# Performance work log

Measured on AMD Instinct MI355X. Metric: run time of the kernel, lower is better.

## Reference

```python
import jax, jax.numpy as jnp
import numpy as np

B, T, E, H, D_PRICE = 16, 2048, 128, 4, 512


def setup_inputs() -> dict:
    key = jax.random.key(0)
    ks = jax.random.split(key, 22)
    f32 = jnp.float32

    def w(k, shape):
        fan_in = shape[0]
        return (jax.random.normal(k, shape, f32) / np.sqrt(fan_in)).astype(f32)

    def b(k, n):
        return (jax.random.normal(k, (n,), f32) * 0.01).astype(f32)

    inp = {
        # OHLC prices, positive, normalized scale
        "ohlc": jax.random.uniform(ks[0], (B, T, 4), f32, 0.5, 1.5),
        # ohlc_proj: Linear(4, 64)
        "Wp": w(ks[1], (4, 64)), "bp": b(ks[2], 64),
        # curvature_net: Linear(64,128) -> ReLU -> Linear(128,32)
        "Wc1": w(ks[3], (64, 128)), "bc1": b(ks[4], 128),
        "Wc2": w(ks[5], (128, 32)), "bc2": b(ks[6], 32),
        # volatility_net: Linear(64,64) -> ReLU -> Linear(64,16)
        "Wv1": w(ks[7], (64, 64)), "bv1": b(ks[8], 64),
        "Wv2": w(ks[9], (64, 16)), "bv2": b(ks[10], 16),
        # sr_field_net: Linear(64,64) -> ReLU -> Linear(64,16)
        "Ws1": w(ks[11], (64, 64)), "bs1": b(ks[12], 64),
        "Ws2": w(ks[13], (64, 16)), "bs2": b(ks[14], 16),
        # MultiheadAttention(embed_dim=128, num_heads=4): fused in-proj + out-proj
        "Wqkv": w(ks[15], (E, 3 * E)), "bqkv": b(ks[16], 3 * E),
        "Wo": w(ks[17], (E, E)), "bo": b(ks[18], E),
        # output_proj: Linear(128, d_price)
        "Wout": w(ks[19], (E, D_PRICE)), "bout": b(ks[20], D_PRICE),
    }
    return inp


def _mlp(x, W1, b1, W2, b2):
    return jax.nn.relu(x @ W1 + b1) @ W2 + b2


def reference(ohlc, Wp, bp, Wc1, bc1, Wc2, bc2, Wv1, bv1, Wv2, bv2,
              Ws1, bs1, Ws2, bs2, Wqkv, bqkv, Wo, bo, Wout, bout):
    # NB: compute_curvature / compute_volatility_surface / detect_sr_levels
    # in the original forward are dead code (results never used), so they are
    # omitted here; output math is identical.
    e = ohlc @ Wp + bp                                   # [B,T,64]
    feats = jnp.concatenate([
        e,
        _mlp(e, Wc1, bc1, Wc2, bc2),                     # [B,T,32]
        _mlp(e, Wv1, bv1, Wv2, bv2),                     # [B,T,16]
        _mlp(e, Ws1, bs1, Ws2, bs2),                     # [B,T,16]
    ], axis=-1)                                          # [B,T,128]

    Bn, Tn, En = feats.shape
    dh = En // H
    qkv = feats @ Wqkv + bqkv                            # [B,T,3E]
    q, k, v = jnp.split(qkv, 3, axis=-1)

    def heads(x):
        return x.reshape(Bn, Tn, H, dh).transpose(0, 2, 1, 3)  # [B,H,T,dh]

    q, k, v = heads(q), heads(k), heads(v)
    scores = jnp.einsum('bhqd,bhkd->bhqk', q, k) / np.sqrt(dh).astype(feats.dtype)
    a = jax.nn.softmax(scores, axis=-1)                  # [B,H,T,T]
    o = jnp.einsum('bhqk,bhkd->bhqd', a, v)
    o = o.transpose(0, 2, 1, 3).reshape(Bn, Tn, En)
    attended = o @ Wo + bo                               # [B,T,128]

    pooled = attended.mean(axis=1)                       # [B,128]
    return pooled @ Wout + bout                          # [B,512]
```

## Files before the change

kernel.cpp:

```cpp
#include <hip/hip_runtime.h>


typedef __attribute__((ext_vector_type(4)))  float f32x4;
typedef __attribute__((ext_vector_type(4)))  short short4v;
typedef __attribute__((ext_vector_type(8)))  short short8v;

static __device__ __forceinline__ unsigned short f2b(float f) {
    unsigned int u = __builtin_bit_cast(unsigned int, f);
    u += 0x7fffu + ((u >> 16) & 1u);
    return (unsigned short)(u >> 16);
}

static __device__ __forceinline__ unsigned int cvtpk_bf16(float a, float b) {
    unsigned int r;
    asm volatile("v_cvt_pk_bf16_f32 %0, %1, %2" : "=v"(r) : "v"(a), "v"(b));
    return r;
}

__global__ __launch_bounds__(256) void prep_kernel(
    const float* Wqkv, const float* Wc1, const float* Wc2, const float* Wv1,
    const float* Wv2, const float* Ws1, const float* Ws2,
    unsigned short* wqkvt, unsigned short* wc1t, unsigned short* wc2t,
    unsigned short* wv1t, unsigned short* wv2t, unsigned short* ws1t,
    unsigned short* ws2t, float* pooled, float* qkmax)
{
    int tid = threadIdx.x;
    if (blockIdx.x < 48) {
        __shared__ float tile[32][33];
        int bidn = blockIdx.x % 12, bidk = blockIdx.x / 12;
        int n0 = bidn * 32, k0 = bidk * 32;
        {
            int r = tid >> 3, cq = tid & 7;
            float4 v = *(const float4*)(Wqkv + (size_t)(k0 + r) * 384 + n0 + cq * 4);
            tile[r][cq*4+0] = v.x; tile[r][cq*4+1] = v.y;
            tile[r][cq*4+2] = v.z; tile[r][cq*4+3] = v.w;
        }
        __syncthreads();
        {
            int nr = tid >> 3, kq = tid & 7;
            union { unsigned short us[4]; short4v v; } pk;
#pragma unroll
            for (int j = 0; j < 4; ++j) pk.us[j] = f2b(tile[kq*4+j][nr]);
            *(short4v*)(wqkvt + (size_t)(n0 + nr) * 128 + k0 + kq * 4) = pk.v;
        }
        return;
    }
    int idx = (blockIdx.x - 48) * 256 + tid;
    if (idx < 8192)  { int n = idx >> 6, kk = idx & 63;  wc1t[idx] = f2b(Wc1[kk*128 + n]); return; }
    idx -= 8192;
    if (idx < 4096)  { int n = idx >> 7, kk = idx & 127; wc2t[idx] = f2b(Wc2[kk*32  + n]); return; }
    idx -= 4096;
    if (idx < 4096)  { int n = idx >> 6, kk = idx & 63;  wv1t[idx] = f2b(Wv1[kk*64  + n]); return; }
    idx -= 4096;
    if (idx < 1024)  { int n = idx >> 6, kk = idx & 63;  wv2t[idx] = f2b(Wv2[kk*16  + n]); return; }
    idx -= 1024;
    if (idx < 4096)  { int n = idx >> 6, kk = idx & 63;  ws1t[idx] = f2b(Ws1[kk*64  + n]); return; }
    idx -= 4096;
    if (idx < 1024)  { int n = idx >> 6, kk = idx & 63;  ws2t[idx] = f2b(Ws2[kk*16  + n]); return; }
    idx -= 1024;
    if (idx < 2048)  { pooled[idx] = 0.f; return; }
    idx -= 2048;
    if (idx < 128)   qkmax[idx] = 0.f;
}

template<int N, int K, int A_ROWB, int D_ROWB, bool RELU, bool TO_LDS>
static __device__ __forceinline__ void tile_gemm(
    const char* As, const unsigned short* __restrict__ BT,
    const float* __restrict__ bias, char* dst,
    unsigned short* __restrict__ gOut, int ocol,
    int m0, int w, int lane)
{
    constexpr int ASL = A_ROWB / 16, DSL = D_ROWB / 16;
    constexpr int NT = N / 16, KS = K / 32;
    int l15 = lane & 15, hi4 = lane >> 4;
    f32x4 acc[NT];
#pragma unroll
    for (int nt = 0; nt < NT; ++nt)
#pragma unroll
        for (int r = 0; r < 4; ++r) acc[nt][r] = 0.f;

#pragma unroll
    for (int ks = 0; ks < KS; ++ks) {
        int slot = ks * 4 + hi4;
        int m = w * 16 + l15;
        short8v af = *(const short8v*)(As + m * A_ROWB + ((slot ^ (m & (ASL - 1))) << 4));
#pragma unroll
        for (int nt = 0; nt < NT; ++nt) {
            int n = nt * 16 + l15;
            short8v bf = *(const short8v*)(BT + (size_t)n * K + slot * 8);
            acc[nt] = __builtin_amdgcn_mfma_f32_16x16x32_bf16(af, bf, acc[nt], 0, 0, 0);
        }
    }
#pragma unroll
    for (int nt = 0; nt < NT; ++nt) {
        int n = nt * 16 + l15;
        float bv = bias[n];
#pragma unroll
        for (int r = 0; r < 4; ++r) {
            int m = w * 16 + hi4 * 4 + r;
            float v = acc[nt][r] + bv;
            if (RELU) v = fmaxf(v, 0.f);
            if (TO_LDS) {
                int col = n;
                *(unsigned short*)(dst + m * D_ROWB + (((col >> 3) ^ (m & (DSL - 1))) << 4) + (col & 7) * 2) = f2b(v);
            } else {
                gOut[(size_t)(m0 + m) * 128 + ocol + n] = f2b(v);
            }
        }
    }
}

__global__ __launch_bounds__(256) void fused_mlp(
    const float* __restrict__ ohlc, const float* __restrict__ Wp, const float* __restrict__ bp,
    const unsigned short* __restrict__ wc1t, const float* __restrict__ bc1,
    const unsigned short* __restrict__ wc2t, const float* __restrict__ bc2,
    const unsigned short* __restrict__ wv1t, const float* __restrict__ bv1,
    const unsigned short* __restrict__ wv2t, const float* __restrict__ bv2,
    const unsigned short* __restrict__ ws1t, const float* __restrict__ bs1,
    const unsigned short* __restrict__ ws2t, const float* __restrict__ bs2,
    unsigned short* __restrict__ feats)
{
    __shared__ float wp[256];
    __shared__ float bpl[64];
    __shared__ char Et[64 * 128];
    __shared__ char Ht[64 * 256];

    int tid = threadIdx.x;
    int m0 = blockIdx.x * 64;
    int branch = blockIdx.y;
    wp[tid] = Wp[tid];
    if (tid < 64) bpl[tid] = bp[tid];
    __syncthreads();

    {
        int tok = tid >> 2, jq = tid & 3;
        float4 ov = ((const float4*)ohlc)[m0 + tok];
#pragma unroll
        for (int c = 0; c < 2; ++c) {
            int sl = jq * 2 + c;
            union { unsigned short us[8]; short8v v; } pk;
#pragma unroll
            for (int jj = 0; jj < 8; ++jj) {
                int j = sl * 8 + jj;
                float e = bpl[j] + ov.x * wp[j] + ov.y * wp[64 + j]
                                 + ov.z * wp[128 + j] + ov.w * wp[192 + j];
                pk.us[jj] = f2b(e);
            }
            *(short8v*)(Et + tok * 128 + ((sl ^ (tok & 7)) << 4)) = pk.v;
            if (branch == 0)
                *(short8v*)(feats + (size_t)(m0 + tok) * 128 + sl * 8) = pk.v;
        }
    }
    __syncthreads();

    int lane = tid & 63, w = tid >> 6;
    if (branch == 0) {
        tile_gemm<128, 64, 128, 256, true, true >(Et, wc1t, bc1, Ht, feats, 0,  m0, w, lane);
        tile_gemm< 32, 128, 256, 256, false, false>(Ht, wc2t, bc2, Ht, feats, 64, m0, w, lane);
    } else if (branch == 1) {
        tile_gemm< 64, 64, 128, 128, true, true >(Et, wv1t, bv1, Ht, feats, 0,  m0, w, lane);
        tile_gemm< 16, 64, 128, 128, false, false>(Ht, wv2t, bv2, Ht, feats, 96, m0, w, lane);
    } else {
        tile_gemm< 64, 64, 128, 128, true, true >(Et, ws1t, bs1, Ht, feats, 0,   m0, w, lane);
        tile_gemm< 16, 64, 128, 128, false, false>(Ht, ws2t, bs2, Ht, feats, 112, m0, w, lane);
    }
}

__global__ __launch_bounds__(256) void qkv_gemm(
    const unsigned short* __restrict__ feats,
    const unsigned short* __restrict__ wqkvt, const float* __restrict__ bqkv,
    unsigned short* __restrict__ qg, unsigned short* __restrict__ kg,
    unsigned short* __restrict__ vt2, float* __restrict__ qkmax)
{
    constexpr int ROWB = 256, CPR = 16;
    __shared__ short8v smemv[4096];
    char* As = (char*)smemv;
    char* Bs = (char*)smemv + 32768;

    int tid = threadIdx.x;
    int m0 = blockIdx.x * 128;
    int sel = blockIdx.y;
    const unsigned short* BT = wqkvt + (size_t)sel * 128 * 128;

    for (int c = tid; c < 128 * CPR; c += 256) {
        int m = c / CPR, s = c % CPR;
        short8v v = *(const short8v*)(feats + (size_t)(m0 + m) * 128 + s * 8);
        *(short8v*)(As + m * ROWB + ((s ^ (m & 15)) * 16)) = v;
    }
    for (int c = tid; c < 128 * CPR; c += 256) {
        int n = c / CPR, s = c % CPR;
        short8v v = *(const short8v*)(BT + (size_t)n * 128 + s * 8);
        *(short8v*)(Bs + n * ROWB + ((s ^ (n & 15)) * 16)) = v;
    }
    __syncthreads();

    int lane = tid & 63, w = tid >> 6;
    int l15 = lane & 15, hi4 = lane >> 4;

    f32x4 acc[2][8];
#pragma unroll
    for (int mt = 0; mt < 2; ++mt)
#pragma unroll
        for (int nt = 0; nt < 8; ++nt)
#pragma unroll
            for (int r = 0; r < 4; ++r) acc[mt][nt][r] = 0.f;

#pragma unroll
    for (int ks = 0; ks < 4; ++ks) {
        int slot = ks * 4 + hi4;
        short8v af[2];
#pragma unroll
        for (int mt = 0; mt < 2; ++mt) {
            int m = w * 32 + mt * 16 + l15;
            af[mt] = *(const short8v*)(As + m * ROWB + ((slot ^ (m & 15)) * 16));
        }
#pragma unroll
        for (int nt = 0; nt < 8; ++nt) {
            int n = nt * 16 + l15;
            short8v bf = *(const short8v*)(Bs + n * ROWB + ((slot ^ (n & 15)) * 16));
            acc[0][nt] = __builtin_amdgcn_mfma_f32_16x16x32_bf16(af[0], bf, acc[0][nt], 0, 0, 0);
            acc[1][nt] = __builtin_amdgcn_mfma_f32_16x16x32_bf16(af[1], bf, acc[1][nt], 0, 0, 0);
        }
    }

    const float QSCALE = 1.4426950408889634f * 0.17677669529663687f;
    int b = m0 >> 11, tp0 = m0 & 2047;

    if (sel == 2) {
#pragma unroll
        for (int mt = 0; mt < 2; ++mt)
#pragma unroll
            for (int nt = 0; nt < 8; ++nt) {
                int n = nt * 16 + l15;
                float bv = bqkv[256 + n];
                int h = n >> 5, dh = n & 31;
                uint2 pk;
                pk.x = cvtpk_bf16(acc[mt][nt][0] + bv, acc[mt][nt][1] + bv);
                pk.y = cvtpk_bf16(acc[mt][nt][2] + bv, acc[mt][nt][3] + bv);
                int g32 = (tp0 >> 5) + w;
                size_t o = (size_t)(b * 4 + h) * 65536 + (size_t)g32 * 1024
                         + dh * 32 + hi4 * 8 + mt * 4;
                *(uint2*)(vt2 + o) = pk;
            }
    } else {
        float amax[4] = {0.f, 0.f, 0.f, 0.f};
        float scale = (sel == 0) ? QSCALE : 1.0f;
#pragma unroll
        for (int mt = 0; mt < 2; ++mt)
#pragma unroll
            for (int nt = 0; nt < 8; ++nt) {
                int n = nt * 16 + l15;
                float bv = bqkv[sel * 128 + n];
#pragma unroll
                for (int r = 0; r < 4; ++r) {
                    float v = (acc[mt][nt][r] + bv) * scale;
                    amax[nt >> 1] = fmaxf(amax[nt >> 1], fabsf(v));
                    int m = w * 32 + mt * 16 + hi4 * 4 + r;
                    *(unsigned short*)(As + m * 256 + (((n >> 3) ^ (m & 7)) << 4) + (n & 7) * 2) = f2b(v);
                }
            }
#pragma unroll
        for (int g = 0; g < 4; ++g) {
            float mv = amax[g];
            mv = fmaxf(mv, __shfl_xor(mv, 1));  mv = fmaxf(mv, __shfl_xor(mv, 2));
            mv = fmaxf(mv, __shfl_xor(mv, 4));  mv = fmaxf(mv, __shfl_xor(mv, 8));
            mv = fmaxf(mv, __shfl_xor(mv, 16)); mv = fmaxf(mv, __shfl_xor(mv, 32));
            if (lane == 0)
                atomicMax((int*)(qkmax + sel * 64 + b * 4 + g), __float_as_int(mv));
        }
        __syncthreads();
        unsigned short* og = (sel == 0) ? qg : kg;
#pragma unroll
        for (int it = 0; it < 8; ++it) {
            int ch = it * 256 + tid;
            int m = ch >> 4, c = ch & 15;
            short8v vv = *(const short8v*)(As + m * 256 + ((c ^ (m & 7)) << 4));
            int h = c >> 2, dq = c & 3;
            *(short8v*)(og + ((size_t)(b * 4 + h) * 2048 + tp0 + m) * 32 + dq * 8) = vv;
        }
    }
}

__global__ __launch_bounds__(256) void attn_kernel(
    const unsigned short* __restrict__ qg, const unsigned short* __restrict__ kg,
    const unsigned short* __restrict__ vt2, const float* __restrict__ qkmax,
    float* __restrict__ pooled)
{
    __shared__ char Kv[2][4096];

    int tid = threadIdx.x, bid = blockIdx.x;
    int bh = bid & 63, qc = bid >> 6;
    int b = bh >> 2;
    int lane = tid & 63, w = tid >> 6;
    int l15 = lane & 15, h = (lane >> 4) & 3;
    int q0 = qc * 128 + w * 32;

    const char* qp = (const char*)qg + ((size_t)bh * 2048 + q0) * 64 + l15 * 64 + h * 16;
    short8v Qf[2];
    Qf[0] = *(const short8v*)(qp);
    Qf[1] = *(const short8v*)(qp + 1024);

    float negM0 = -(32.0f * qkmax[bh] * qkmax[64 + bh]);
    f32x4 NEGM4 = {negM0, negM0, negM0, negM0};

    f32x4 accO[2][2], lacc[2];
#pragma unroll
    for (int j = 0; j < 2; ++j)
#pragma unroll
        for (int r = 0; r < 4; ++r) { accO[j][0][r] = 0.f; accO[j][1][r] = 0.f; lacc[j][r] = 0.f; }

    short8v ONES;
    {
        union { unsigned short us[8]; short8v v; } u;
#pragma unroll
        for (int j = 0; j < 8; ++j) u.us[j] = 0x3F80;
        ONES = u.v;
    }

    const char* gk = (const char*)kg  + (size_t)bh * 131072;
    const char* gv = (const char*)vt2 + (size_t)bh * 131072;
    const char* gsrc = (tid < 128) ? (gk + tid * 16) : (gv + (tid - 128) * 16);
    int ldst = tid * 16;
    int foff = l15 * 64 + h * 16;

    auto compute = [&](const char* bufp) {
        short8v Ka = *(const short8v*)(bufp + foff);
        short8v Kb = *(const short8v*)(bufp + 1024 + foff);
        short8v Va = *(const short8v*)(bufp + 2048 + foff);
        short8v Vb = *(const short8v*)(bufp + 3072 + foff);
        union { unsigned int u[4]; short8v v; } pk[2];
#pragma unroll
        for (int tau = 0; tau < 2; ++tau) {
            short8v Kf = tau ? Kb : Ka;
#pragma unroll
            for (int j = 0; j < 2; ++j) {
                f32x4 s = __builtin_amdgcn_mfma_f32_16x16x32_bf16(Kf, Qf[j], NEGM4, 0, 0, 0);
                float p0 = __builtin_amdgcn_exp2f(s[0]);
                float p1 = __builtin_amdgcn_exp2f(s[1]);
                float p2 = __builtin_amdgcn_exp2f(s[2]);
                float p3 = __builtin_amdgcn_exp2f(s[3]);
                pk[j].u[tau * 2 + 0] = cvtpk_bf16(p0, p1);
                pk[j].u[tau * 2 + 1] = cvtpk_bf16(p2, p3);
            }
        }
#pragma unroll
        for (int j = 0; j < 2; ++j) {
            lacc[j]    = __builtin_amdgcn_mfma_f32_16x16x32_bf16(ONES, pk[j].v, lacc[j], 0, 0, 0);
            accO[j][0] = __builtin_amdgcn_mfma_f32_16x16x32_bf16(Va,   pk[j].v, accO[j][0], 0, 0, 0);
            accO[j][1] = __builtin_amdgcn_mfma_f32_16x16x32_bf16(Vb,   pk[j].v, accO[j][1], 0, 0, 0);
        }
    };

    short8v R;
    R = *(const short8v*)(gsrc);
    *(short8v*)(Kv[0] + ldst) = R;
    R = *(const short8v*)(gsrc + 2048);
    __syncthreads();

#pragma unroll 1
    for (int g = 0; g < 64; g += 2) {
        *(short8v*)(Kv[1] + ldst) = R;
        if (g + 2 < 64) R = *(const short8v*)(gsrc + (size_t)(g + 2) * 2048);
        compute(Kv[0]);
        __syncthreads();
        if (g + 2 < 64) *(short8v*)(Kv[0] + ldst) = R;
        if (g + 3 < 64) R = *(const short8v*)(gsrc + (size_t)(g + 3) * 2048);
        compute(Kv[1]);
        __syncthreads();
    }

    float o8[2][4];
#pragma unroll
    for (int d = 0; d < 2; ++d)
#pragma unroll
        for (int r = 0; r < 4; ++r) o8[d][r] = 0.f;
#pragma unroll
    for (int j = 0; j < 2; ++j) {
        float inv = 1.0f / (lacc[j][0] + 1e-30f);
#pragma unroll
        for (int d = 0; d < 2; ++d)
#pragma unroll
            for (int r = 0; r < 4; ++r) o8[d][r] += accO[j][d][r] * inv;
    }
#pragma unroll
    for (int d = 0; d < 2; ++d)
#pragma unroll
        for (int r = 0; r < 4; ++r) {
            float v = o8[d][r];
            v += __shfl_xor(v, 1); v += __shfl_xor(v, 2);
            v += __shfl_xor(v, 4); v += __shfl_xor(v, 8);
            if (l15 == 0) {
                int dh = d * 16 + h * 4 + r;
                atomicAdd(pooled + b * 128 + (bh & 3) * 32 + dh, v);
            }
        }
}

__global__ __launch_bounds__(256) void head_kernel(
    const float* __restrict__ pooled, const float* __restrict__ Wo,
    const float* __restrict__ bo, const float* __restrict__ Wout,
    const float* __restrict__ bout, float* __restrict__ out)
{
    int bq = blockIdx.x, tid = threadIdx.x;
    __shared__ float pl[128], mid[128];
    if (tid < 128) pl[tid] = pooled[bq * 128 + tid] * (1.f / 2048.f);
    __syncthreads();
    if (tid < 128) {
        float s = bo[tid];
#pragma unroll 4
        for (int c = 0; c < 128; ++c) s += pl[c] * Wo[c * 128 + tid];
        mid[tid] = s;
    }
    __syncthreads();
    for (int j = tid; j < 512; j += 256) {
        float s = bout[j];
#pragma unroll 4
        for (int i = 0; i < 128; ++i) s += mid[i] * Wout[i * 512 + j];
        out[bq * 512 + j] = s;
    }
}

extern "C" void kernel_launch(void* const* d_in, const int* in_sizes, int n_in,
                              void* d_out, int out_size, void* d_ws, size_t ws_size,
                              hipStream_t stream) {
    (void)in_sizes; (void)n_in; (void)out_size; (void)ws_size;
    const float* ohlc = (const float*)d_in[0];
    const float* Wp   = (const float*)d_in[1];  const float* bp   = (const float*)d_in[2];
    const float* Wc1  = (const float*)d_in[3];  const float* bc1  = (const float*)d_in[4];
    const float* Wc2  = (const float*)d_in[5];  const float* bc2  = (const float*)d_in[6];
    const float* Wv1  = (const float*)d_in[7];  const float* bv1  = (const float*)d_in[8];
    const float* Wv2  = (const float*)d_in[9];  const float* bv2  = (const float*)d_in[10];
    const float* Ws1  = (const float*)d_in[11]; const float* bs1  = (const float*)d_in[12];
    const float* Ws2  = (const float*)d_in[13]; const float* bs2  = (const float*)d_in[14];
    const float* Wqkv = (const float*)d_in[15]; const float* bqkv = (const float*)d_in[16];
    const float* Wo   = (const float*)d_in[17]; const float* bo   = (const float*)d_in[18];
    const float* Wout = (const float*)d_in[19]; const float* bout = (const float*)d_in[20];
    float* out = (float*)d_out;
    char* ws = (char*)d_ws;

    const size_t MB8 = 8388608;
    unsigned short* feats = (unsigned short*)(ws);
    unsigned short* qg    = (unsigned short*)(ws + 1 * MB8);
    unsigned short* kg    = (unsigned short*)(ws + 2 * MB8);
    unsigned short* vt2   = (unsigned short*)(ws + 3 * MB8);
    float*          pooled = (float*)(ws + 4 * MB8);
    float*          qkmax  = (float*)(ws + 4 * MB8 + 8192);
    unsigned short* wc1t  = (unsigned short*)(ws + 4 * MB8 + 8192 + 512);
    unsigned short* wc2t  = wc1t + 8192;
    unsigned short* wv1t  = wc2t + 4096;
    unsigned short* wv2t  = wv1t + 4096;
    unsigned short* ws1t  = wv2t + 1024;
    unsigned short* ws2t  = ws1t + 4096;
    unsigned short* wqkvt = ws2t + 1024;

    prep_kernel<<<145, 256, 0, stream>>>(Wqkv, Wc1, Wc2, Wv1, Wv2, Ws1, Ws2,
                                         wqkvt, wc1t, wc2t, wv1t, wv2t, ws1t, ws2t,
                                         pooled, qkmax);
    fused_mlp<<<dim3(512, 3), 256, 0, stream>>>(ohlc, Wp, bp, wc1t, bc1, wc2t, bc2,
                                                wv1t, bv1, wv2t, bv2, ws1t, bs1, ws2t, bs2, feats);
    qkv_gemm<<<dim3(256, 3), 256, 0, stream>>>(feats, wqkvt, bqkv, qg, kg, vt2, qkmax);
    attn_kernel<<<1024, 256, 0, stream>>>(qg, kg, vt2, qkmax, pooled);
    head_kernel<<<16, 256, 0, stream>>>(pooled, Wo, bo, Wout, bout, out);
}
```

Measured before the change: 134.7 us.

## Stage MLP weights in LDS, raise MFMA priority, peel attention loop tail

The MLP kernel now copies each branch's transposed bf16 weights into shared memory once per block, overlapped with the embedding computation. The tile GEMMs then read B fragments from swizzled LDS instead of global memory, and one barrier is removed by merging the weight staging with the existing sync. The attention loop raises wave priority with s_setprio around its MFMA/exp compute. It also drops the per-iteration bounds checks by peeling the final iteration and advancing a running pointer. Extra LDS use (24KB) may lower occupancy in the MLP kernel.

```diff
diff --git a/kernel.cpp b/kernel.cpp
--- a/kernel.cpp
+++ b/kernel.cpp
@@ -63,14 +63,25 @@
     if (idx < 128)   qkmax[idx] = 0.f;
 }
 
+template<int N, int K>
+static __device__ __forceinline__ void stage_w(
+    const unsigned short* __restrict__ wt, char* Bs, int tid)
+{
+    constexpr int SL = K / 8;
+#pragma unroll
+    for (int c = tid; c < N * SL; c += 256) {
+        int n = c / SL, s = c % SL;
+        short8v v = *(const short8v*)(wt + n * K + s * 8);
+        *(short8v*)(Bs + n * (K * 2) + ((s ^ (n & (SL - 1))) << 4)) = v;
+    }
+}
+
 template<int N, int K, int A_ROWB, int D_ROWB, bool RELU, bool TO_LDS>
-static __device__ __forceinline__ void tile_gemm(
-    const char* As, const unsigned short* __restrict__ BT,
-    const float* __restrict__ bias, char* dst,
-    unsigned short* __restrict__ gOut, int ocol,
-    int m0, int w, int lane)
-{
-    constexpr int ASL = A_ROWB / 16, DSL = D_ROWB / 16;
+static __device__ __forceinline__ void tile_gemm_l(
+    const char* As, const char* Bs, const float* __restrict__ bias, char* dst,
+    unsigned short* __restrict__ gOut, int ocol, int m0, int w, int lane)
+{
+    constexpr int ASL = A_ROWB / 16, DSL = D_ROWB / 16, BSL = K / 8;
     constexpr int NT = N / 16, KS = K / 32;
     int l15 = lane & 15, hi4 = lane >> 4;
     f32x4 acc[NT];
@@ -87,7 +98,7 @@
 #pragma unroll
         for (int nt = 0; nt < NT; ++nt) {
             int n = nt * 16 + l15;
-            short8v bf = *(const short8v*)(BT + (size_t)n * K + slot * 8);
+            short8v bf = *(const short8v*)(Bs + n * (K * 2) + ((slot ^ (n & (BSL - 1))) << 4));
             acc[nt] = __builtin_amdgcn_mfma_f32_16x16x32_bf16(af, bf, acc[nt], 0, 0, 0);
         }
     }
@@ -101,8 +112,7 @@
             float v = acc[nt][r] + bv;
             if (RELU) v = fmaxf(v, 0.f);
             if (TO_LDS) {
-                int col = n;
-                *(unsigned short*)(dst + m * D_ROWB + (((col >> 3) ^ (m & (DSL - 1))) << 4) + (col & 7) * 2) = f2b(v);
+                *(unsigned short*)(dst + m * D_ROWB + (((n >> 3) ^ (m & (DSL - 1))) << 4) + (n & 7) * 2) = f2b(v);
             } else {
                 gOut[(size_t)(m0 + m) * 128 + ocol + n] = f2b(v);
             }
@@ -124,12 +134,18 @@
     __shared__ float bpl[64];
     __shared__ char Et[64 * 128];
     __shared__ char Ht[64 * 256];
+    __shared__ char Bw1[16384];
+    __shared__ char Bw2[8192];
 
     int tid = threadIdx.x;
     int m0 = blockIdx.x * 64;
     int branch = blockIdx.y;
     wp[tid] = Wp[tid];
     if (tid < 64) bpl[tid] = bp[tid];
+
+    if (branch == 0)      { stage_w<128, 64>(wc1t, Bw1, tid); stage_w<32, 128>(wc2t, Bw2, tid); }
+    else if (branch == 1) { stage_w< 64, 64>(wv1t, Bw1, tid); stage_w<16,  64>(wv2t, Bw2, tid); }
+    else                  { stage_w< 64, 64>(ws1t, Bw1, tid); stage_w<16,  64>(ws2t, Bw2, tid); }
     __syncthreads();
 
     {
@@ -151,18 +167,17 @@
                 *(short8v*)(feats + (size_t)(m0 + tok) * 128 + sl * 8) = pk.v;
         }
     }
-    __syncthreads();
 
     int lane = tid & 63, w = tid >> 6;
     if (branch == 0) {
-        tile_gemm<128, 64, 128, 256, true, true >(Et, wc1t, bc1, Ht, feats, 0,  m0, w, lane);
-        tile_gemm< 32, 128, 256, 256, false, false>(Ht, wc2t, bc2, Ht, feats, 64, m0, w, lane);
+        tile_gemm_l<128, 64, 128, 256, true, true >(Et, Bw1, bc1, Ht, feats, 0,  m0, w, lane);
+        tile_gemm_l< 32, 128, 256, 256, false, false>(Ht, Bw2, bc2, Ht, feats, 64, m0, w, lane);
     } else if (branch == 1) {
-        tile_gemm< 64, 64, 128, 128, true, true >(Et, wv1t, bv1, Ht, feats, 0,  m0, w, lane);
-        tile_gemm< 16, 64, 128, 128, false, false>(Ht, wv2t, bv2, Ht, feats, 96, m0, w, lane);
+        tile_gemm_l< 64, 64, 128, 128, true, true >(Et, Bw1, bv1, Ht, feats, 0,  m0, w, lane);
+        tile_gemm_l< 16, 64, 128, 128, false, false>(Ht, Bw2, bv2, Ht, feats, 96, m0, w, lane);
     } else {
-        tile_gemm< 64, 64, 128, 128, true, true >(Et, ws1t, bs1, Ht, feats, 0,   m0, w, lane);
-        tile_gemm< 16, 64, 128, 128, false, false>(Ht, ws2t, bs2, Ht, feats, 112, m0, w, lane);
+        tile_gemm_l< 64, 64, 128, 128, true, true >(Et, Bw1, bs1, Ht, feats, 0,   m0, w, lane);
+        tile_gemm_l< 16, 64, 128, 128, false, false>(Ht, Bw2, bs2, Ht, feats, 112, m0, w, lane);
     }
 }
 
@@ -328,6 +343,7 @@
         short8v Kb = *(const short8v*)(bufp + 1024 + foff);
         short8v Va = *(const short8v*)(bufp + 2048 + foff);
         short8v Vb = *(const short8v*)(bufp + 3072 + foff);
+        __builtin_amdgcn_s_setprio(1);
         union { unsigned int u[4]; short8v v; } pk[2];
 #pragma unroll
         for (int tau = 0; tau < 2; ++tau) {
@@ -349,6 +365,7 @@
             accO[j][0] = __builtin_amdgcn_mfma_f32_16x16x32_bf16(Va,   pk[j].v, accO[j][0], 0, 0, 0);
             accO[j][1] = __builtin_amdgcn_mfma_f32_16x16x32_bf16(Vb,   pk[j].v, accO[j][1], 0, 0, 0);
         }
+        __builtin_amdgcn_s_setprio(0);
     };
 
     short8v R;
@@ -357,17 +374,23 @@
     R = *(const short8v*)(gsrc + 2048);
     __syncthreads();
 
+    const char* gp = gsrc + 2 * 2048;
 #pragma unroll 1
-    for (int g = 0; g < 64; g += 2) {
+    for (int g = 0; g < 62; g += 2) {
         *(short8v*)(Kv[1] + ldst) = R;
-        if (g + 2 < 64) R = *(const short8v*)(gsrc + (size_t)(g + 2) * 2048);
+        short8v R2 = *(const short8v*)(gp);
         compute(Kv[0]);
         __syncthreads();
-        if (g + 2 < 64) *(short8v*)(Kv[0] + ldst) = R;
-        if (g + 3 < 64) R = *(const short8v*)(gsrc + (size_t)(g + 3) * 2048);
+        *(short8v*)(Kv[0] + ldst) = R2;
+        R = *(const short8v*)(gp + 2048);
+        gp += 4096;
         compute(Kv[1]);
         __syncthreads();
     }
+    *(short8v*)(Kv[1] + ldst) = R;
+    compute(Kv[0]);
+    __syncthreads();
+    compute(Kv[1]);
 
     float o8[2][4];
 #pragma unroll
```

After: 130.5 us. -3.1%, faster.
